# Optimization experiments

Measured on AMD Instinct MI355X. Metric: run time of the kernel, lower is better.

Reference implementation:

```python
import jax, jax.numpy as jnp
import numpy as np

N, D = 8192, 768
EPS = 1e-5  # torch LayerNorm default


def setup_inputs() -> dict:
    key = jax.random.key(0)
    ks = jax.random.split(key, 5)
    q = jax.random.normal(ks[0], (N, D), dtype=jnp.float32)
    k = jax.random.normal(ks[1], (N, D), dtype=jnp.float32)
    v = jax.random.normal(ks[2], (N, D), dtype=jnp.float32)
    ln_w = jnp.ones((D,), dtype=jnp.float32)
    ln_b = jnp.zeros((D,), dtype=jnp.float32)
    W_qkv = jax.random.normal(ks[3], (D, D), dtype=jnp.float32) * 0.02
    W_proj = jax.random.normal(ks[4], (D, D), dtype=jnp.float32) * 0.02
    b_proj = jnp.zeros((D,), dtype=jnp.float32)
    return {"q": q, "k": k, "v": v, "ln_w": ln_w, "ln_b": ln_b,
            "W_qkv": W_qkv, "W_proj": W_proj, "b_proj": b_proj}


def reference(q, k, v, ln_w, ln_b, W_qkv, W_proj, b_proj):
    dim = q.shape[-1]
    scale = dim ** (-0.5)

    def ln(x):
        mu = jnp.mean(x, axis=-1, keepdims=True)
        var = jnp.mean((x - mu) ** 2, axis=-1, keepdims=True)
        return (x - mu) * jax.lax.rsqrt(var + EPS) * ln_w + ln_b

    # shared LayerNorm + shared Linear (toto0, no bias) applied to q, k, v
    qn = ln(q) @ W_qkv.T  # [N, D]
    kn = ln(k) @ W_qkv.T
    vn = ln(v) @ W_qkv.T

    attn = jnp.einsum('qc,kc->qk', qn, kn) * scale  # [N, N]
    attn = jax.nn.softmax(attn, axis=-1)
    out = jnp.einsum('qk,kc->qc', attn, vn)  # [N, D]
    out = out @ W_proj.T + b_proj  # proj0
    return out
```

## Files before the change

kernel.cpp:

```cpp
#include <hip/hip_runtime.h>
#include <hip/hip_bf16.h>
#include <stdint.h>

typedef short bf16x8 __attribute__((ext_vector_type(8)));
typedef float f32x4 __attribute__((ext_vector_type(4)));
typedef unsigned short u16;
typedef u16 u16x8 __attribute__((ext_vector_type(8)));

__device__ __forceinline__ u16 f2bf(float x) {
  __hip_bfloat16 h = __float2bfloat16(x);
  return *reinterpret_cast<u16*>(&h);
}
__device__ __forceinline__ float bf2f(u16 v) {
  unsigned u = (unsigned)v << 16;
  return *reinterpret_cast<float*>(&u);
}

__device__ __forceinline__ void gload_lds16(const void* g, const void* lds_base) {
  __builtin_amdgcn_global_load_lds(
      (const __attribute__((address_space(1))) unsigned int*)(uintptr_t)g,
      (__attribute__((address_space(3))) unsigned int*)(uintptr_t)lds_base,
      16, 0, 0);
}

#define BAR() __builtin_amdgcn_s_barrier()

__global__ __launch_bounds__(256) void ln_cast_kernel(
    const float* __restrict__ q, const float* __restrict__ k, const float* __restrict__ v,
    const float* __restrict__ lw, const float* __restrict__ lb, u16* __restrict__ out) {
  int row = blockIdx.x;
  const float* x;
  if (row < 8192) x = q + (size_t)row * 768;
  else if (row < 16384) x = k + (size_t)(row - 8192) * 768;
  else x = v + (size_t)(row - 16384) * 768;
  int t = threadIdx.x;
  float a0 = x[t], a1 = x[t + 256], a2 = x[t + 512];
  __shared__ float red[4];
  __shared__ float red2[4];
  float s = a0 + a1 + a2;
  for (int o = 32; o; o >>= 1) s += __shfl_down(s, o, 64);
  if ((t & 63) == 0) red[t >> 6] = s;
  __syncthreads();
  float mean = (red[0] + red[1] + red[2] + red[3]) * (1.0f / 768.0f);
  float d0 = a0 - mean, d1 = a1 - mean, d2 = a2 - mean;
  float vs = d0 * d0 + d1 * d1 + d2 * d2;
  for (int o = 32; o; o >>= 1) vs += __shfl_down(vs, o, 64);
  if ((t & 63) == 0) red2[t >> 6] = vs;
  __syncthreads();
  float var = (red2[0] + red2[1] + red2[2] + red2[3]) * (1.0f / 768.0f);
  float rstd = rsqrtf(var + 1e-5f);
  u16* o_ = out + (size_t)row * 768;
  o_[t]       = f2bf(d0 * rstd * lw[t]       + lb[t]);
  o_[t + 256] = f2bf(d1 * rstd * lw[t + 256] + lb[t + 256]);
  o_[t + 512] = f2bf(d2 * rstd * lw[t + 512] + lb[t + 512]);
}

__global__ __launch_bounds__(256) void cast_f32_bf16(const float* __restrict__ in,
                                                     u16* __restrict__ out, int n4) {
  int i = blockIdx.x * 256 + threadIdx.x;
  if (i < n4) {
    float4 vv = ((const float4*)in)[i];
    ushort4 o;
    o.x = f2bf(vv.x); o.y = f2bf(vv.y); o.z = f2bf(vv.z); o.w = f2bf(vv.w);
    ((ushort4*)out)[i] = o;
  }
}

__global__ __launch_bounds__(256) void zero_f32(float* __restrict__ p, int n) {
  int i = blockIdx.x * 256 + threadIdx.x;
  if (i < n) p[i] = 0.0f;
}

__global__ __launch_bounds__(256) void transpose64(const u16* __restrict__ in, u16* __restrict__ out) {
  __shared__ __align__(16) u16 tile[64][72];
  int b = blockIdx.x;
  int tr = b / 12, tc = b % 12;
  int t = threadIdx.x;
  int r = t >> 3;
  int cb = (t & 7) << 3;
#pragma unroll
  for (int i = 0; i < 2; i++) {
    int row = r + i * 32;
    const u16* src = in + (size_t)(tr * 64 + row) * 768 + tc * 64 + cb;
    *(uint4*)&tile[row][cb] = *(const uint4*)src;
  }
  __syncthreads();
#pragma unroll
  for (int i = 0; i < 2; i++) {
    int oc = r + i * 32;
    u16x8 tmp;
#pragma unroll
    for (int j = 0; j < 8; j++) tmp[j] = tile[cb + j][oc];
    u16* dst = out + (size_t)(tc * 64 + oc) * 8192 + tr * 64 + cb;
    *(u16x8*)dst = tmp;
  }
}

__global__ __launch_bounds__(256) void reduce4_scale(
    const u16* __restrict__ p0, const u16* __restrict__ p1,
    const u16* __restrict__ p2, const u16* __restrict__ p3,
    const float* __restrict__ rowsum, u16* __restrict__ out, int n8) {
  int i = blockIdx.x * 256 + threadIdx.x;
  if (i < n8) {
    float inv = 1.0f / rowsum[i / 96];
    u16x8 a = ((const u16x8*)p0)[i];
    u16x8 b = ((const u16x8*)p1)[i];
    u16x8 c = ((const u16x8*)p2)[i];
    u16x8 d = ((const u16x8*)p3)[i];
    u16x8 o;
#pragma unroll
    for (int j = 0; j < 8; j++)
      o[j] = f2bf((bf2f(a[j]) + bf2f(b[j]) + bf2f(c[j]) + bf2f(d[j])) * inv);
    ((u16x8*)out)[i] = o;
  }
}

__global__ __launch_bounds__(512, 2) void qk_exp_256(
    const u16* __restrict__ A, const u16* __restrict__ B, u16* __restrict__ C,
    float* __restrict__ rowsum, float scale) {
  __shared__ __align__(16) u16 sA[4][256 * 32];
  __shared__ __align__(16) u16 sB[4][256 * 32];
  int orig = blockIdx.x;
  int xcd = orig & 7, i = orig >> 3;
  int tm = xcd * 4 + (i & 3), tn = i >> 2;
  const int t = threadIdx.x, l = t & 63, w = t >> 6;
  const int wr = w >> 2, wc = w & 3;
  const int lr = l & 15, lq = l >> 4;
  const int colb = lq * 16;

  f32x4 acc[8][4];
#pragma unroll
  for (int m = 0; m < 8; m++)
#pragma unroll
    for (int n = 0; n < 4; n++) acc[m][n] = (f32x4){0.f, 0.f, 0.f, 0.f};

  const size_t rA0 = (size_t)tm * 256, rB0 = (size_t)tn * 256;

  auto SCALL = [&](int b, int Tn, int idx) {
    const u16* src = (idx < 2) ? A : B;
    size_t r0 = (idx < 2) ? rA0 : rB0;
    char* dst = (char*)((idx < 2) ? sA[b] : sB[b]);
    int p = idx & 1;
    int x = p * 8192 + t * 16;
    int r = x >> 6;
    int cb = (x & 63) ^ (((r >> 1) & 3) << 4);
    gload_lds16((const char*)(src + (r0 + r) * 768 + (Tn << 5)) + cb,
                dst + p * 8192 + w * 1024);
  };
  auto LOADA = [&](bf16x8 (&aF)[4], int d, int mh) {
#pragma unroll
    for (int mf = 0; mf < 4; mf++) {
      int row = wr * 128 + (mh * 4 + mf) * 16 + lr;
      int x = row * 64 + colb;
      aF[mf] = *(const bf16x8*)((const char*)sA[d] + (x ^ (((row >> 1) & 3) << 4)));
    }
  };
  auto LOADB = [&](bf16x8 (&bF)[4], int d) {
#pragma unroll
    for (int nf = 0; nf < 4; nf++) {
      int row = wc * 64 + nf * 16 + lr;
      int x = row * 64 + colb;
      bF[nf] = *(const bf16x8*)((const char*)sB[d] + (x ^ (((row >> 1) & 3) << 4)));
    }
  };
  auto MM = [&](bf16x8 (&aF)[4], bf16x8 (&bF)[4], int mh) {
    __builtin_amdgcn_s_setprio(1);
#pragma unroll
    for (int mf = 0; mf < 4; mf++)
#pragma unroll
      for (int nf = 0; nf < 4; nf++)
        acc[mh * 4 + mf][nf] = __builtin_amdgcn_mfma_f32_16x16x32_bf16(
            aF[mf], bF[nf], acc[mh * 4 + mf][nf], 0, 0, 0);
    __builtin_amdgcn_s_setprio(0);
  };

#pragma unroll
  for (int idx = 0; idx < 4; idx++) SCALL(0, 0, idx);
#pragma unroll
  for (int idx = 0; idx < 4; idx++) SCALL(1, 1, idx);
  asm volatile("s_waitcnt vmcnt(4)" ::: "memory");
  BAR();

#pragma unroll 4
  for (int T = 0; T < 24; T++) {
    const int cur = T & 3;
    bf16x8 aF[4], bF[4];
    LOADA(aF, cur, 0);
    LOADB(bF, cur);
    if (T + 2 < 24) {
      const int nb = (T + 2) & 3;
      SCALL(nb, T + 2, 0); SCALL(nb, T + 2, 1);
      SCALL(nb, T + 2, 2); SCALL(nb, T + 2, 3);
    }
    BAR();
    MM(aF, bF, 0);
    bf16x8 aG[4];
    LOADA(aG, cur, 1);
    MM(aG, bF, 1);
    if (T < 22) { asm volatile("s_waitcnt vmcnt(4)" ::: "memory"); }
    else        { asm volatile("s_waitcnt vmcnt(0)" ::: "memory"); }
    BAR();
  }

  float rs[8][4];
#pragma unroll
  for (int m = 0; m < 8; m++)
#pragma unroll
    for (int j = 0; j < 4; j++) rs[m][j] = 0.0f;
  const size_t rowBase = rA0 + (size_t)wr * 128;
  const int colBase = tn * 256 + wc * 64;
#pragma unroll
  for (int mi = 0; mi < 8; mi++) {
    size_t row0 = rowBase + mi * 16 + lq * 4;
#pragma unroll
    for (int nf = 0; nf < 4; nf++) {
      int col = colBase + nf * 16 + lr;
#pragma unroll
      for (int j = 0; j < 4; j++) {
        float e = __expf(acc[mi][nf][j] * scale);
        C[(row0 + j) * 8192 + col] = f2bf(e);
        rs[mi][j] += e;
      }
    }
  }
#pragma unroll
  for (int mi = 0; mi < 8; mi++)
#pragma unroll
    for (int j = 0; j < 4; j++) {
      float r = rs[mi][j];
      r += __shfl_xor(r, 1); r += __shfl_xor(r, 2);
      r += __shfl_xor(r, 4); r += __shfl_xor(r, 8);
      if (lr == 0) atomicAdd(&rowsum[rowBase + mi * 16 + lq * 4 + j], r);
    }
}

template <int MODE>
__global__ __launch_bounds__(256, 2) void gemm_bt(
    const u16* __restrict__ A0, const u16* __restrict__ B0,
    void* __restrict__ Cv0, void* __restrict__ Cv1,
    int M, int N, int K, int lda, int ldb, int ldc,
    float scale, const float* __restrict__ bias, size_t cSplitStride) {
  __shared__ __align__(16) u16 sA[128 * 64];
  __shared__ __align__(16) u16 sB[128 * 64];
  const int z = blockIdx.y;
  const u16* A = A0 + (size_t)z * (size_t)K;
  const u16* B = B0 + (size_t)z * (size_t)K;
  u16* Cb = (z < 2) ? ((u16*)Cv0 + (size_t)z * cSplitStride)
                    : ((u16*)Cv1 + (size_t)(z - 2) * cSplitStride);
  const int nTn = N >> 7;
  int nwg = gridDim.x, orig = blockIdx.x;
  int qq = nwg >> 3, rr = nwg & 7;
  int xcd = orig & 7, loc = orig >> 3;
  int wg = (xcd < rr ? xcd * (qq + 1) : rr * (qq + 1) + (xcd - rr) * qq) + loc;
  int tm = wg / nTn, tn = wg % nTn;

  const int t = threadIdx.x, l = t & 63, w = t >> 6;
  const int wr = w >> 1, wc = w & 1;
  const int lr = l & 15, kg = (l >> 4) << 3;

  f32x4 acc[4][4];
#pragma unroll
  for (int m = 0; m < 4; m++)
#pragma unroll
    for (int n = 0; n < 4; n++) acc[m][n] = (f32x4){0.f, 0.f, 0.f, 0.f};

  const size_t rowA0 = (size_t)tm * 128;
  const size_t rowB0 = (size_t)tn * 128;
  const int nk = K >> 6;
  for (int kt = 0; kt < nk; kt++) {
    const int k0 = kt << 6;
#pragma unroll
    for (int i = 0; i < 4; i++) {
      int chunk = i * 256 + t;
      int row = chunk >> 3;
      int col = (chunk & 7) << 3;
      gload_lds16(A + (rowA0 + row) * lda + k0 + col, (const char*)sA + (i * 256 + w * 64) * 16);
      gload_lds16(B + (rowB0 + row) * ldb + k0 + col, (const char*)sB + (i * 256 + w * 64) * 16);
    }
    __syncthreads();
#pragma unroll
    for (int kk = 0; kk < 2; kk++) {
      bf16x8 af[4], bfv[4];
#pragma unroll
      for (int m = 0; m < 4; m++)
        af[m] = *(const bf16x8*)&sA[(wr * 64 + m * 16 + lr) * 64 + kk * 32 + kg];
#pragma unroll
      for (int n = 0; n < 4; n++)
        bfv[n] = *(const bf16x8*)&sB[(wc * 64 + n * 16 + lr) * 64 + kk * 32 + kg];
#pragma unroll
      for (int m = 0; m < 4; m++)
#pragma unroll
        for (int n = 0; n < 4; n++)
          acc[m][n] = __builtin_amdgcn_mfma_f32_16x16x32_bf16(af[m], bfv[n], acc[m][n], 0, 0, 0);
    }
    __syncthreads();
  }
#pragma unroll
  for (int m = 0; m < 4; m++) {
    int row = tm * 128 + wr * 64 + m * 16 + ((l >> 4) << 2);
#pragma unroll
    for (int n = 0; n < 4; n++) {
      int col = tn * 128 + wc * 64 + n * 16 + lr;
#pragma unroll
      for (int j = 0; j < 4; j++) {
        float vl = acc[m][n][j];
        if (MODE == 0) Cb[(size_t)(row + j) * ldc + col] = f2bf(vl * scale);
        else ((float*)Cv0)[(size_t)(row + j) * ldc + col] = vl + bias[col];
      }
    }
  }
}

extern "C" void kernel_launch(void* const* d_in, const int* in_sizes, int n_in,
                              void* d_out, int out_size, void* d_ws, size_t ws_size,
                              hipStream_t stream) {
  const float* q  = (const float*)d_in[0];
  const float* k  = (const float*)d_in[1];
  const float* v  = (const float*)d_in[2];
  const float* lw = (const float*)d_in[3];
  const float* lb = (const float*)d_in[4];
  const float* Wq = (const float*)d_in[5];
  const float* Wp = (const float*)d_in[6];
  const float* bp = (const float*)d_in[7];

  char* ws = (char*)d_ws;
  size_t off = 0;
  auto alloc = [&](size_t b) { size_t o = off; off += (b + 255) & ~(size_t)255; return o; };
  size_t o_ln = alloc((size_t)24576 * 768 * 2);
  size_t o_pj = alloc((size_t)24576 * 768 * 2);
  size_t o_wq = alloc((size_t)768 * 768 * 2);
  size_t o_wp = alloc((size_t)768 * 768 * 2);
  u16* lnbuf = (u16*)(ws + o_ln);
  u16* pj    = (u16*)(ws + o_pj);
  u16* wqb   = (u16*)(ws + o_wq);
  u16* wpb   = (u16*)(ws + o_wp);
  const size_t NS = (size_t)8192 * 768;
  u16* vnT = lnbuf;
  u16* p0  = lnbuf + NS;
  u16* p1  = lnbuf + 2 * NS;
  float* rowsum = (float*)(pj + 2 * NS);
  u16* p2 = (u16*)d_out;
  u16* p3 = p2 + NS;
  size_t fixedEnd = off;
  u16* Sbuf = (u16*)(ws + fixedEnd);

  const float scale = 0.03608439182435161f;

  ln_cast_kernel<<<dim3(24576), dim3(256), 0, stream>>>(q, k, v, lw, lb, lnbuf);
  cast_f32_bf16<<<dim3(576), dim3(256), 0, stream>>>(Wq, wqb, 147456);
  cast_f32_bf16<<<dim3(576), dim3(256), 0, stream>>>(Wp, wpb, 147456);

  gemm_bt<0><<<dim3(1152), dim3(256), 0, stream>>>(lnbuf, wqb, (void*)pj, (void*)pj,
      24576, 768, 768, 768, 768, 768, 1.0f, (const float*)nullptr, 0);

  transpose64<<<dim3(1536), dim3(256), 0, stream>>>(pj + (size_t)16384 * 768, vnT);
  zero_f32<<<dim3(32), dim3(256), 0, stream>>>(rowsum, 8192);

  qk_exp_256<<<dim3(1024), dim3(512), 0, stream>>>(pj, pj + NS, Sbuf, rowsum, scale);

  gemm_bt<0><<<dim3(384, 4), dim3(256), 0, stream>>>(
      Sbuf, vnT, (void*)p0, (void*)p2,
      8192, 768, 2048, 8192, 8192, 768, 1.0f, (const float*)nullptr, NS);

  reduce4_scale<<<dim3(3072), dim3(256), 0, stream>>>(p0, p1, p2, p3, rowsum, p0, (int)(NS / 8));

  gemm_bt<2><<<dim3(384), dim3(256), 0, stream>>>(p0, wpb, d_out, d_out,
      8192, 768, 768, 768, 768, 768, 1.0f, bp, 0);
}
```

Before: 362.5 us.

## Deepen QK-exp GEMM prefetch to three stages with precomputed LDS offsets

Reworks the QK^T+exp kernel's main loop so global-to-LDS loads run three tiles ahead instead of two, using all four LDS buffers with an explicit unrolled phase schedule and vmcnt(8) waits. The global source pointers and swizzled LDS read offsets are computed once before the loop, and the two shared arrays become one flat buffer. The aim is to hide more global-load latency and cut per-iteration address arithmetic, at the cost of more in-flight loads, a more complex hand-written schedule and possibly more register pressure.

```diff
diff --git a/kernel.cpp b/kernel.cpp
--- a/kernel.cpp
+++ b/kernel.cpp
@@ -118,8 +118,7 @@
 __global__ __launch_bounds__(512, 2) void qk_exp_256(
     const u16* __restrict__ A, const u16* __restrict__ B, u16* __restrict__ C,
     float* __restrict__ rowsum, float scale) {
-  __shared__ __align__(16) u16 sA[4][256 * 32];
-  __shared__ __align__(16) u16 sB[4][256 * 32];
+  __shared__ __align__(16) u16 lds[8 * 256 * 32];
   int orig = blockIdx.x;
   int xcd = orig & 7, i = orig >> 3;
   int tm = xcd * 4 + (i & 3), tn = i >> 2;
@@ -136,32 +135,48 @@
 
   const size_t rA0 = (size_t)tm * 256, rB0 = (size_t)tn * 256;
 
-  auto SCALL = [&](int b, int Tn, int idx) {
+  const char* gsrc[4];
+  int ldsoff[4];
+#pragma unroll
+  for (int idx = 0; idx < 4; idx++) {
     const u16* src = (idx < 2) ? A : B;
     size_t r0 = (idx < 2) ? rA0 : rB0;
-    char* dst = (char*)((idx < 2) ? sA[b] : sB[b]);
     int p = idx & 1;
     int x = p * 8192 + t * 16;
     int r = x >> 6;
     int cb = (x & 63) ^ (((r >> 1) & 3) << 4);
-    gload_lds16((const char*)(src + (r0 + r) * 768 + (Tn << 5)) + cb,
-                dst + p * 8192 + w * 1024);
-  };
-  auto LOADA = [&](bf16x8 (&aF)[4], int d, int mh) {
+    gsrc[idx] = (const char*)(src + (r0 + r) * 768) + cb;
+    ldsoff[idx] = ((idx < 2) ? 0 : 65536) + p * 8192 + w * 1024;
+  }
+  int offA[2][4], offB[4];
+#pragma unroll
+  for (int mh = 0; mh < 2; mh++)
 #pragma unroll
     for (int mf = 0; mf < 4; mf++) {
       int row = wr * 128 + (mh * 4 + mf) * 16 + lr;
       int x = row * 64 + colb;
-      aF[mf] = *(const bf16x8*)((const char*)sA[d] + (x ^ (((row >> 1) & 3) << 4)));
-    }
+      offA[mh][mf] = x ^ (((row >> 1) & 3) << 4);
+    }
+#pragma unroll
+  for (int nf = 0; nf < 4; nf++) {
+    int row = wc * 64 + nf * 16 + lr;
+    int x = row * 64 + colb;
+    offB[nf] = 65536 + (x ^ (((row >> 1) & 3) << 4));
+  }
+
+#define SCALL(BUF, TT, IDX)                                                  \
+  gload_lds16(gsrc[IDX] + (size_t)(TT) * 64,                                 \
+              (const char*)lds + (BUF) * 16384 + ldsoff[IDX])
+
+  auto LOADA = [&](bf16x8 (&aF)[4], int b, int mh) {
+#pragma unroll
+    for (int mf = 0; mf < 4; mf++)
+      aF[mf] = *(const bf16x8*)((const char*)lds + b * 16384 + offA[mh][mf]);
   };
-  auto LOADB = [&](bf16x8 (&bF)[4], int d) {
-#pragma unroll
-    for (int nf = 0; nf < 4; nf++) {
-      int row = wc * 64 + nf * 16 + lr;
-      int x = row * 64 + colb;
-      bF[nf] = *(const bf16x8*)((const char*)sB[d] + (x ^ (((row >> 1) & 3) << 4)));
-    }
+  auto LOADB = [&](bf16x8 (&bF)[4], int b) {
+#pragma unroll
+    for (int nf = 0; nf < 4; nf++)
+      bF[nf] = *(const bf16x8*)((const char*)lds + b * 16384 + offB[nf]);
   };
   auto MM = [&](bf16x8 (&aF)[4], bf16x8 (&bF)[4], int mh) {
     __builtin_amdgcn_s_setprio(1);
@@ -174,33 +189,44 @@
     __builtin_amdgcn_s_setprio(0);
   };
 
-#pragma unroll
-  for (int idx = 0; idx < 4; idx++) SCALL(0, 0, idx);
-#pragma unroll
-  for (int idx = 0; idx < 4; idx++) SCALL(1, 1, idx);
-  asm volatile("s_waitcnt vmcnt(4)" ::: "memory");
+#define PHASE(CUR, SBUF, STAGET, DOSTAGE, VMN)                               \
+  do {                                                                       \
+    bf16x8 aF[4], bF[4], aG[4];                                              \
+    LOADA(aF, CUR, 0);                                                       \
+    LOADB(bF, CUR);                                                          \
+    if (DOSTAGE) {                                                           \
+      SCALL(SBUF, STAGET, 0); SCALL(SBUF, STAGET, 1);                        \
+      SCALL(SBUF, STAGET, 2); SCALL(SBUF, STAGET, 3);                        \
+    }                                                                        \
+    BAR();                                                                   \
+    MM(aF, bF, 0);                                                           \
+    LOADA(aG, CUR, 1);                                                       \
+    MM(aG, bF, 1);                                                           \
+    if ((VMN) == 8) asm volatile("s_waitcnt vmcnt(8)" ::: "memory");         \
+    else if ((VMN) == 4) asm volatile("s_waitcnt vmcnt(4)" ::: "memory");    \
+    else if ((VMN) == 0) asm volatile("s_waitcnt vmcnt(0)" ::: "memory");    \
+    BAR();                                                                   \
+  } while (0)
+
+  SCALL(0, 0, 0); SCALL(0, 0, 1); SCALL(0, 0, 2); SCALL(0, 0, 3);
+  SCALL(1, 1, 0); SCALL(1, 1, 1); SCALL(1, 1, 2); SCALL(1, 1, 3);
+  SCALL(2, 2, 0); SCALL(2, 2, 1); SCALL(2, 2, 2); SCALL(2, 2, 3);
+  asm volatile("s_waitcnt vmcnt(8)" ::: "memory");
   BAR();
 
-#pragma unroll 4
-  for (int T = 0; T < 24; T++) {
-    const int cur = T & 3;
-    bf16x8 aF[4], bF[4];
-    LOADA(aF, cur, 0);
-    LOADB(bF, cur);
-    if (T + 2 < 24) {
-      const int nb = (T + 2) & 3;
-      SCALL(nb, T + 2, 0); SCALL(nb, T + 2, 1);
-      SCALL(nb, T + 2, 2); SCALL(nb, T + 2, 3);
-    }
-    BAR();
-    MM(aF, bF, 0);
-    bf16x8 aG[4];
-    LOADA(aG, cur, 1);
-    MM(aG, bF, 1);
-    if (T < 22) { asm volatile("s_waitcnt vmcnt(4)" ::: "memory"); }
-    else        { asm volatile("s_waitcnt vmcnt(0)" ::: "memory"); }
-    BAR();
-  }
+  for (int Tb = 0; Tb < 20; Tb += 4) {
+    PHASE(0, 3, Tb + 3, 1, 8);
+    PHASE(1, 0, Tb + 4, 1, 8);
+    PHASE(2, 1, Tb + 5, 1, 8);
+    PHASE(3, 2, Tb + 6, 1, 8);
+  }
+  PHASE(0, 3, 23, 1, 8);
+  PHASE(1, 0, 0, 0, 4);
+  PHASE(2, 0, 0, 0, 0);
+  PHASE(3, 0, 0, 0, -1);
+
+#undef PHASE
+#undef SCALL
 
   float rs[8][4];
 #pragma unroll
```

New measurement: 359.4 us. About the same (-0.8%).
